# Kernel optimization log

Hardware: AMD Instinct MI355X
Metric: run time of the kernel (lower is better)

The kernel has to match this reference:

```python
import jax, jax.numpy as jnp
import numpy as np

D_MODEL, N_HEADS, D_HEAD, N_CTX, BATCH = 1024, 16, 64, 2048, 4
SCALED = True
NEG = 1e10


def setup_inputs() -> dict:
    key = jax.random.key(0)
    k1, k2, k3, k4 = jax.random.split(key, 4)
    s = 1.0 / np.sqrt(D_MODEL)
    return {
        "x": jax.random.normal(k1, (BATCH, N_CTX, D_MODEL), dtype=jnp.float32),
        "W_K": jax.random.normal(k2, (N_HEADS, D_HEAD, D_MODEL), dtype=jnp.float32) * s,
        "W_Q": jax.random.normal(k3, (N_HEADS, D_HEAD, D_MODEL), dtype=jnp.float32) * s,
        "W_V": jax.random.normal(k4, (N_HEADS, D_HEAD, D_MODEL), dtype=jnp.float32) * s,
    }


def reference(x, W_K, W_Q, W_V):
    b, p, _ = x.shape
    k = jnp.einsum('ihd,bpd->biph', W_K, x)
    q = jnp.einsum('ihd,bpd->biph', W_Q, x)
    v = jnp.einsum('ihd,bpd->biph', W_V, x)
    # attn_scores_pre: [b, i, q, p] (query axis named q, key axis p)
    scores = jnp.einsum('biph,biqh->biqp', k, q)
    mask = jnp.tril(jnp.ones((p, p), dtype=scores.dtype))
    scores = jnp.tril(scores) - NEG * (1.0 - mask)
    if SCALED:
        scores = scores / np.sqrt(D_HEAD)
    attn = jax.nn.softmax(scores, axis=-1)
    z = jnp.einsum('biph,biqp->biqh', v, attn)  # [b, i, q, h]
    out = jnp.transpose(z, (0, 2, 1, 3)).reshape(b, p, -1)  # b q (i h)
    return out
```

## Files before the change

### kernel.cpp

```cpp
#include <hip/hip_runtime.h>
#include <stdint.h>

typedef unsigned short u16;
typedef short bf16x8 __attribute__((ext_vector_type(8)));
typedef float f32x4 __attribute__((ext_vector_type(4)));
typedef u16 u16x8 __attribute__((ext_vector_type(8)));
typedef u16 u16x4 __attribute__((ext_vector_type(4)));
typedef uint32_t u32x2 __attribute__((ext_vector_type(2)));

#define NB 4
#define NH 16
#define NP 2048
#define NDM 1024
#define NEGBIG (-1e30f)
#define KLOG2E 0.18033688011112042f

__device__ __forceinline__ u16 f2bf(float f) {
    union { float f; uint32_t u; } v; v.f = f;
    return (u16)((v.u + 0x7FFFu + ((v.u >> 16) & 1u)) >> 16);
}

__device__ __forceinline__ uint32_t cvtpk_bf16(float lo, float hi) {
    uint32_t r;
    asm("v_cvt_pk_bf16_f32 %0, %1, %2" : "=v"(r) : "v"(lo), "v"(hi));
    return r;
}

__global__ void convert_x(const float* __restrict__ src, u16* __restrict__ dst, int n) {
    int i = (blockIdx.x * blockDim.x + threadIdx.x) * 4;
    int stride = gridDim.x * blockDim.x * 4;
    for (; i < n; i += stride) {
        float4 f = *(const float4*)(src + i);
        u16x4 o = { f2bf(f.x), f2bf(f.y), f2bf(f.z), f2bf(f.w) };
        *(u16x4*)(dst + i) = o;
    }
}

__global__ void convert_w(const float* __restrict__ wq, const float* __restrict__ wk,
                          const float* __restrict__ wv, u16* __restrict__ dst) {
    const int M = 1024 * 1024;
    int i = (blockIdx.x * blockDim.x + threadIdx.x) * 4;
    const float* src;
    float scale;
    if (i < M)            { src = wq + i;         scale = KLOG2E; }
    else if (i < 2 * M)   { src = wk + (i - M);   scale = 1.0f; }
    else                  { src = wv + (i - 2*M); scale = 1.0f; }
    float4 f = *(const float4*)src;
    u16x4 o = { f2bf(f.x * scale), f2bf(f.y * scale), f2bf(f.z * scale), f2bf(f.w * scale) };
    *(u16x4*)(dst + i) = o;
}

__device__ __forceinline__ void load_lds16(const void* g, void* l) {
    __builtin_amdgcn_global_load_lds(
        (const __attribute__((address_space(1))) uint32_t*)g,
        (__attribute__((address_space(3))) uint32_t*)l,
        16, 0, 0);
}

__global__ __launch_bounds__(256) void proj_gemm(
    const u16* __restrict__ xbf, const u16* __restrict__ wbf,
    u16* __restrict__ qws, u16* __restrict__ kws, u16* __restrict__ vtmp)
{
    __shared__ u16 As[128 * 64];
    __shared__ u16 Bs[128 * 64];
    int tid = threadIdx.x;
    int wave = tid >> 6, lane = tid & 63;
    int g = lane >> 4, c = lane & 15;
    int wr = wave >> 1, wc = wave & 1;
    int gx = blockIdx.x, gy = blockIdx.y;
    int wsel = gy >> 3;
    int n0 = (gy & 7) * 128;
    long m0 = (long)gx * 128;
    const u16* asrc0 = xbf + m0 * 1024;
    const u16* bsrc0 = wbf + (long)wsel * (1024 * 1024) + (long)n0 * 1024;

    int lrow = lane >> 3;
    int lcol = (lane & 7) * 8;

    f32x4 acc[4][4];
    #pragma unroll
    for (int i = 0; i < 4; i++)
        #pragma unroll
        for (int j = 0; j < 4; j++) acc[i][j] = (f32x4){0.f, 0.f, 0.f, 0.f};

    for (int kt = 0; kt < 16; kt++) {
        const u16* ak = asrc0 + kt * 64;
        const u16* bk_ = bsrc0 + kt * 64;
        #pragma unroll
        for (int r = 0; r < 4; r++) {
            int ldsoff = r * 2048 + wave * 512;
            int grow = r * 32 + wave * 8 + lrow;
            load_lds16(ak + (long)grow * 1024 + lcol, &As[ldsoff]);
            load_lds16(bk_ + (long)grow * 1024 + lcol, &Bs[ldsoff]);
        }
        __syncthreads();
        #pragma unroll
        for (int ks = 0; ks < 2; ks++) {
            bf16x8 af[4], bf_[4];
            #pragma unroll
            for (int mt = 0; mt < 4; mt++)
                af[mt] = *(const bf16x8*)&As[(wr * 64 + mt * 16 + c) * 64 + ks * 32 + g * 8];
            #pragma unroll
            for (int nt = 0; nt < 4; nt++)
                bf_[nt] = *(const bf16x8*)&Bs[(wc * 64 + nt * 16 + c) * 64 + ks * 32 + g * 8];
            #pragma unroll
            for (int mt = 0; mt < 4; mt++)
                #pragma unroll
                for (int nt = 0; nt < 4; nt++)
                    acc[mt][nt] = __builtin_amdgcn_mfma_f32_16x16x32_bf16(bf_[nt], af[mt], acc[mt][nt], 0, 0, 0);
        }
        __syncthreads();
    }

    u16* dst = (wsel == 0) ? qws : (wsel == 1) ? kws : vtmp;
    #pragma unroll
    for (int mt = 0; mt < 4; mt++) {
        #pragma unroll
        for (int nt = 0; nt < 4; nt++) {
            long m = m0 + wr * 64 + mt * 16 + c;
            int n_base = n0 + wc * 64 + nt * 16 + g * 4;
            int b = (int)(m >> 11), p = (int)(m & 2047);
            int hd = n_base >> 6, h = n_base & 63;
            u16x4 o;
            #pragma unroll
            for (int r = 0; r < 4; r++) o[r] = f2bf(acc[mt][nt][r]);
            *(u16x4*)(dst + ((((long)b * NH + hd) * NP + p) << 6) + h) = o;
        }
    }
}

__global__ __launch_bounds__(256) void transpose_v(const u16* __restrict__ src, u16* __restrict__ dst) {
    __shared__ u16 t[64][80];
    int tid = threadIdx.x;
    int bh = blockIdx.y;
    int p0 = blockIdx.x * 64;
    const u16* s = src + ((long)bh * NP + p0) * 64;
    #pragma unroll
    for (int rep = 0; rep < 2; rep++) {
        int pr = rep * 32 + (tid >> 3);
        int cc = (tid & 7) * 8;
        *(u16x8*)&t[pr][cc] = *(const u16x8*)(s + pr * 64 + cc);
    }
    __syncthreads();
    u16* d = dst + (long)bh * 64 * NP + p0;
    #pragma unroll
    for (int rep = 0; rep < 2; rep++) {
        int dh = rep * 32 + (tid >> 3);
        int pc = (tid & 7) * 8;
        u16x8 o;
        #pragma unroll
        for (int j = 0; j < 8; j++) o[j] = t[pc + j][dh];
        *(u16x8*)(d + (long)dh * NP + pc) = o;
    }
}

template<bool MASK>
__device__ __forceinline__ void attn_tile_lds(
    int kv0, const uint8_t* ldsK, const uint8_t* ldsV,
    const bf16x8 (&aq)[2][2], uint8_t* PwB, int c, int g, int q0,
    f32x4 (&acc_o)[2][4], float (&lrow)[2])
{
    int g4 = g * 4;
    int swz = (c & 7) << 4;

    f32x4 sa[2][4];
    __builtin_amdgcn_s_setprio(1);
    #pragma unroll
    for (int a = 0; a < 4; a++) {
        bf16x8 kf0 = *(const bf16x8*)(ldsK + (a * 16 + c) * 128 + ((g * 16) ^ swz));
        bf16x8 kf1 = *(const bf16x8*)(ldsK + (a * 16 + c) * 128 + ((64 + g * 16) ^ swz));
        #pragma unroll
        for (int mt = 0; mt < 2; mt++) {
            f32x4 z = (f32x4){0.f, 0.f, 0.f, 0.f};
            z = __builtin_amdgcn_mfma_f32_16x16x32_bf16(kf0, aq[mt][0], z, 0, 0, 0);
            z = __builtin_amdgcn_mfma_f32_16x16x32_bf16(kf1, aq[mt][1], z, 0, 0, 0);
            sa[mt][a] = z;
        }
    }
    __builtin_amdgcn_s_setprio(0);

    #pragma unroll
    for (int mt = 0; mt < 2; mt++) {
        float ps = 0.f;
        #pragma unroll
        for (int a = 0; a < 4; a++) {
            float p[4];
            #pragma unroll
            for (int r = 0; r < 4; r++) {
                p[r] = __builtin_amdgcn_exp2f(sa[mt][a][r] - 8.0f);
                if (MASK) {
                    int key = kv0 + a * 16 + g4 + r;
                    int qq = q0 + mt * 16 + c;
                    if (key > qq) p[r] = 0.f;
                }
                ps += p[r];
            }
            u32x2 wd = { cvtpk_bf16(p[0], p[1]), cvtpk_bf16(p[2], p[3]) };
            *(u32x2*)(PwB + c * 128 + ((a * 32 + g * 8) ^ swz)) = wd;
        }
        ps += __shfl_xor(ps, 16);
        ps += __shfl_xor(ps, 32);
        lrow[mt] += ps;

        __builtin_amdgcn_wave_barrier();

        __builtin_amdgcn_s_setprio(1);
        #pragma unroll
        for (int s = 0; s < 2; s++) {
            bf16x8 pa = *(const bf16x8*)(PwB + c * 128 + ((s * 64 + g * 16) ^ swz));
            #pragma unroll
            for (int j = 0; j < 4; j++) {
                bf16x8 bv = *(const bf16x8*)(ldsV + (j * 16 + c) * 128 + ((s * 64 + g * 16) ^ swz));
                acc_o[mt][j] = __builtin_amdgcn_mfma_f32_16x16x32_bf16(pa, bv, acc_o[mt][j], 0, 0, 0);
            }
        }
        __builtin_amdgcn_s_setprio(0);
        __builtin_amdgcn_wave_barrier();
    }
}

__global__ __launch_bounds__(512, 4) void attn_kernel(
    const u16* __restrict__ qws, const u16* __restrict__ kws,
    const u16* __restrict__ vT, float* __restrict__ out)
{
    __shared__ __align__(16) uint8_t smem[65536];
    int tid = threadIdx.x;
    int wave = tid >> 6, lane = tid & 63;
    int c = lane & 15, g = lane >> 4;
    int xs = blockIdx.x >> 6;
    int qb = (xs < 4) ? (7 - 2 * xs) : (2 * (xs - 4));
    int bh = blockIdx.x & 63;
    int q0 = qb * 256 + wave * 32;
    const u16* qp = qws + (long)bh * NP * 64;
    const uint8_t* kb = (const uint8_t*)(kws + (long)bh * NP * 64);
    const uint8_t* vb = (const uint8_t*)(vT + (long)bh * 64 * NP);
    uint8_t* PwB = smem + 49152 + wave * 2048;

    bf16x8 aq[2][2];
    #pragma unroll
    for (int mt = 0; mt < 2; mt++)
        #pragma unroll
        for (int s = 0; s < 2; s++)
            aq[mt][s] = *(const bf16x8*)(qp + (long)(q0 + mt * 16 + c) * 64 + s * 32 + g * 8);

    f32x4 acc_o[2][4];
    float lrow[2] = {0.f, 0.f};
    #pragma unroll
    for (int mt = 0; mt < 2; mt++)
        #pragma unroll
        for (int j = 0; j < 4; j++) acc_o[mt][j] = (f32x4){0.f, 0.f, 0.f, 0.f};

    int r3 = lane >> 3;
    int cb = ((lane & 7) ^ r3) << 4;
    int srow = wave * 8 + r3;

    int myTmax = (q0 + 31) >> 6;
    int Tblk = qb * 4 + 3;

    auto stage = [&](int t) {
        uint8_t* dst = smem + (t % 3) * 16384;
        int kv = t * 64;
        load_lds16(kb + (size_t)(kv + srow) * 128 + cb, dst + wave * 1024);
        load_lds16(vb + (size_t)srow * (NP * 2) + (size_t)kv * 2 + cb, dst + 8192 + wave * 1024);
    };

    stage(0);
    stage(1);
    asm volatile("s_waitcnt vmcnt(2)" ::: "memory");
    __builtin_amdgcn_sched_barrier(0);
    __builtin_amdgcn_s_barrier();
    __builtin_amdgcn_sched_barrier(0);

    for (int t = 0; t <= Tblk; t++) {
        if (t + 2 <= Tblk) stage(t + 2);
        if (t <= myTmax) {
            const uint8_t* ldsK = smem + (t % 3) * 16384;
            const uint8_t* ldsV = ldsK + 8192;
            if (t == myTmax)
                attn_tile_lds<true>(t * 64, ldsK, ldsV, aq, PwB, c, g, q0, acc_o, lrow);
            else
                attn_tile_lds<false>(t * 64, ldsK, ldsV, aq, PwB, c, g, q0, acc_o, lrow);
        }
        asm volatile("s_waitcnt vmcnt(2)" ::: "memory");
        __builtin_amdgcn_sched_barrier(0);
        __builtin_amdgcn_s_barrier();
        __builtin_amdgcn_sched_barrier(0);
    }

    int b = bh >> 4, hh = bh & 15;
    #pragma unroll
    for (int mt = 0; mt < 2; mt++) {
        float invc = 1.0f / lrow[mt];
        #pragma unroll
        for (int r = 0; r < 4; r++) {
            float li = __shfl(invc, g * 4 + r);
            int qq = q0 + mt * 16 + g * 4 + r;
            #pragma unroll
            for (int j = 0; j < 4; j++)
                out[((long)b * NP + qq) * 1024 + hh * 64 + j * 16 + c] = acc_o[mt][j][r] * li;
        }
    }
}

extern "C" void kernel_launch(void* const* d_in, const int* in_sizes, int n_in,
                              void* d_out, int out_size, void* d_ws, size_t ws_size,
                              hipStream_t stream) {
    const float* x  = (const float*)d_in[0];
    const float* wk = (const float*)d_in[1];
    const float* wq = (const float*)d_in[2];
    const float* wv = (const float*)d_in[3];

    uint8_t* ws = (uint8_t*)d_ws;
    u16* x_bf  = (u16*)(ws + 0);
    u16* w_bf  = (u16*)(ws + (16u << 20));
    u16* q_ws  = (u16*)(ws + (22u << 20));
    u16* k_ws  = (u16*)(ws + (38u << 20));
    u16* vtmp  = (u16*)(ws + (54u << 20));
    u16* v_wsT = (u16*)(ws + 0);

    convert_x<<<2048, 256, 0, stream>>>(x, x_bf, NB * NP * NDM);
    convert_w<<<3072, 256, 0, stream>>>(wq, wk, wv, w_bf);

    proj_gemm<<<dim3(64, 24), 256, 0, stream>>>(x_bf, w_bf, q_ws, k_ws, vtmp);
    transpose_v<<<dim3(32, 64), 256, 0, stream>>>(vtmp, v_wsT);
    attn_kernel<<<512, 512, 0, stream>>>(q_ws, k_ws, v_wsT, (float*)d_out);
}
```

Baseline: 189.3 us.

## Fuse conversions, write V transposed from GEMM, and load attention K/V from global

The two fp32→bf16 conversion kernels are merged into a single launch. The V projection epilogue now writes V already transposed, so the separate transpose kernel goes away. The attention kernel drops its shared-memory triple-buffered K/V pipeline: each wave reads K and V straight from global memory and keeps only a per-wave P buffer with a new swizzle. Blocks shrink to 4 waves over 128 query rows with a new causal balancing order. This cuts launches and a V round trip, but adds scalar, uncoalesced V stores in the GEMM and loses K/V reuse across waves in LDS.

Result: slower. 227.5 us (+20.2%).

```diff
diff --git a/kernel.cpp b/kernel.cpp
--- a/kernel.cpp
+++ b/kernel.cpp
@@ -12,7 +12,6 @@
 #define NH 16
 #define NP 2048
 #define NDM 1024
-#define NEGBIG (-1e30f)
 #define KLOG2E 0.18033688011112042f
 
 __device__ __forceinline__ u16 f2bf(float f) {
@@ -26,28 +25,24 @@
     return r;
 }
 
-__global__ void convert_x(const float* __restrict__ src, u16* __restrict__ dst, int n) {
+__global__ void convert_all(const float* __restrict__ x, const float* __restrict__ wq,
+                            const float* __restrict__ wk, const float* __restrict__ wv,
+                            u16* __restrict__ x_bf, u16* __restrict__ w_bf) {
+    const int XT = NB * NP * NDM;
+    const int M1 = NDM * NDM;
     int i = (blockIdx.x * blockDim.x + threadIdx.x) * 4;
-    int stride = gridDim.x * blockDim.x * 4;
-    for (; i < n; i += stride) {
-        float4 f = *(const float4*)(src + i);
-        u16x4 o = { f2bf(f.x), f2bf(f.y), f2bf(f.z), f2bf(f.w) };
-        *(u16x4*)(dst + i) = o;
-    }
-}
-
-__global__ void convert_w(const float* __restrict__ wq, const float* __restrict__ wk,
-                          const float* __restrict__ wv, u16* __restrict__ dst) {
-    const int M = 1024 * 1024;
-    int i = (blockIdx.x * blockDim.x + threadIdx.x) * 4;
-    const float* src;
-    float scale;
-    if (i < M)            { src = wq + i;         scale = KLOG2E; }
-    else if (i < 2 * M)   { src = wk + (i - M);   scale = 1.0f; }
-    else                  { src = wv + (i - 2*M); scale = 1.0f; }
+    const float* src; u16* dst; float scale = 1.0f;
+    if (i < XT) { src = x + i; dst = x_bf + i; }
+    else {
+        int j = i - XT;
+        dst = w_bf + j;
+        if (j < M1)          { src = wq + j;          scale = KLOG2E; }
+        else if (j < 2 * M1) { src = wk + (j - M1); }
+        else                 { src = wv + (j - 2 * M1); }
+    }
     float4 f = *(const float4*)src;
     u16x4 o = { f2bf(f.x * scale), f2bf(f.y * scale), f2bf(f.z * scale), f2bf(f.w * scale) };
-    *(u16x4*)(dst + i) = o;
+    *(u16x4*)dst = o;
 }
 
 __device__ __forceinline__ void load_lds16(const void* g, void* l) {
@@ -59,7 +54,7 @@
 
 __global__ __launch_bounds__(256) void proj_gemm(
     const u16* __restrict__ xbf, const u16* __restrict__ wbf,
-    u16* __restrict__ qws, u16* __restrict__ kws, u16* __restrict__ vtmp)
+    u16* __restrict__ qws, u16* __restrict__ kws, u16* __restrict__ vT)
 {
     __shared__ u16 As[128 * 64];
     __shared__ u16 Bs[128 * 64];
@@ -112,129 +107,124 @@
         __syncthreads();
     }
 
-    u16* dst = (wsel == 0) ? qws : (wsel == 1) ? kws : vtmp;
-    #pragma unroll
-    for (int mt = 0; mt < 4; mt++) {
-        #pragma unroll
-        for (int nt = 0; nt < 4; nt++) {
+    if (wsel < 2) {
+        u16* dst = (wsel == 0) ? qws : kws;
+        #pragma unroll
+        for (int mt = 0; mt < 4; mt++) {
+            #pragma unroll
+            for (int nt = 0; nt < 4; nt++) {
+                long m = m0 + wr * 64 + mt * 16 + c;
+                int n_base = n0 + wc * 64 + nt * 16 + g * 4;
+                int b = (int)(m >> 11), p = (int)(m & 2047);
+                int hd = n_base >> 6, h = n_base & 63;
+                u16x4 o;
+                #pragma unroll
+                for (int r = 0; r < 4; r++) o[r] = f2bf(acc[mt][nt][r]);
+                *(u16x4*)(dst + ((((long)b * NH + hd) * NP + p) << 6) + h) = o;
+            }
+        }
+    } else {
+        #pragma unroll
+        for (int mt = 0; mt < 4; mt++) {
             long m = m0 + wr * 64 + mt * 16 + c;
-            int n_base = n0 + wc * 64 + nt * 16 + g * 4;
             int b = (int)(m >> 11), p = (int)(m & 2047);
-            int hd = n_base >> 6, h = n_base & 63;
-            u16x4 o;
-            #pragma unroll
-            for (int r = 0; r < 4; r++) o[r] = f2bf(acc[mt][nt][r]);
-            *(u16x4*)(dst + ((((long)b * NH + hd) * NP + p) << 6) + h) = o;
-        }
-    }
-}
-
-__global__ __launch_bounds__(256) void transpose_v(const u16* __restrict__ src, u16* __restrict__ dst) {
-    __shared__ u16 t[64][80];
-    int tid = threadIdx.x;
-    int bh = blockIdx.y;
-    int p0 = blockIdx.x * 64;
-    const u16* s = src + ((long)bh * NP + p0) * 64;
-    #pragma unroll
-    for (int rep = 0; rep < 2; rep++) {
-        int pr = rep * 32 + (tid >> 3);
-        int cc = (tid & 7) * 8;
-        *(u16x8*)&t[pr][cc] = *(const u16x8*)(s + pr * 64 + cc);
-    }
-    __syncthreads();
-    u16* d = dst + (long)bh * 64 * NP + p0;
-    #pragma unroll
-    for (int rep = 0; rep < 2; rep++) {
-        int dh = rep * 32 + (tid >> 3);
-        int pc = (tid & 7) * 8;
-        u16x8 o;
-        #pragma unroll
-        for (int j = 0; j < 8; j++) o[j] = t[pc + j][dh];
-        *(u16x8*)(d + (long)dh * NP + pc) = o;
+            #pragma unroll
+            for (int nt = 0; nt < 4; nt++) {
+                int n_base = n0 + wc * 64 + nt * 16 + g * 4;
+                #pragma unroll
+                for (int r = 0; r < 4; r++)
+                    vT[((long)b * 1024 + n_base + r) * NP + p] = f2bf(acc[mt][nt][r]);
+            }
+        }
     }
 }
 
 template<bool MASK>
-__device__ __forceinline__ void attn_tile_lds(
-    int kv0, const uint8_t* ldsK, const uint8_t* ldsV,
-    const bf16x8 (&aq)[2][2], uint8_t* PwB, int c, int g, int q0,
+__device__ __forceinline__ void attn_tile(
+    int kv0, const u16* __restrict__ kp, const u16* __restrict__ vp,
+    const bf16x8 (&aq)[2][2], uint8_t* PwB, int c, int g, int sx, int q0,
     f32x4 (&acc_o)[2][4], float (&lrow)[2])
 {
-    int g4 = g * 4;
-    int swz = (c & 7) << 4;
-
-    f32x4 sa[2][4];
-    __builtin_amdgcn_s_setprio(1);
+    float ps[2] = {0.f, 0.f};
     #pragma unroll
     for (int a = 0; a < 4; a++) {
-        bf16x8 kf0 = *(const bf16x8*)(ldsK + (a * 16 + c) * 128 + ((g * 16) ^ swz));
-        bf16x8 kf1 = *(const bf16x8*)(ldsK + (a * 16 + c) * 128 + ((64 + g * 16) ^ swz));
+        const u16* kr = kp + (size_t)(kv0 + a * 16 + c) * 64 + g * 8;
+        bf16x8 kf0 = *(const bf16x8*)(kr);
+        bf16x8 kf1 = *(const bf16x8*)(kr + 32);
         #pragma unroll
         for (int mt = 0; mt < 2; mt++) {
             f32x4 z = (f32x4){0.f, 0.f, 0.f, 0.f};
             z = __builtin_amdgcn_mfma_f32_16x16x32_bf16(kf0, aq[mt][0], z, 0, 0, 0);
             z = __builtin_amdgcn_mfma_f32_16x16x32_bf16(kf1, aq[mt][1], z, 0, 0, 0);
-            sa[mt][a] = z;
-        }
-    }
-    __builtin_amdgcn_s_setprio(0);
-
-    #pragma unroll
-    for (int mt = 0; mt < 2; mt++) {
-        float ps = 0.f;
-        #pragma unroll
-        for (int a = 0; a < 4; a++) {
             float p[4];
             #pragma unroll
             for (int r = 0; r < 4; r++) {
-                p[r] = __builtin_amdgcn_exp2f(sa[mt][a][r] - 8.0f);
+                p[r] = __builtin_amdgcn_exp2f(z[r] - 8.0f);
                 if (MASK) {
-                    int key = kv0 + a * 16 + g4 + r;
+                    int key = kv0 + a * 16 + g * 4 + r;
                     int qq = q0 + mt * 16 + c;
                     if (key > qq) p[r] = 0.f;
                 }
-                ps += p[r];
+                ps[mt] += p[r];
             }
             u32x2 wd = { cvtpk_bf16(p[0], p[1]), cvtpk_bf16(p[2], p[3]) };
-            *(u32x2*)(PwB + c * 128 + ((a * 32 + g * 8) ^ swz)) = wd;
-        }
-        ps += __shfl_xor(ps, 16);
-        ps += __shfl_xor(ps, 32);
-        lrow[mt] += ps;
-
-        __builtin_amdgcn_wave_barrier();
-
-        __builtin_amdgcn_s_setprio(1);
-        #pragma unroll
-        for (int s = 0; s < 2; s++) {
-            bf16x8 pa = *(const bf16x8*)(PwB + c * 128 + ((s * 64 + g * 16) ^ swz));
-            #pragma unroll
-            for (int j = 0; j < 4; j++) {
-                bf16x8 bv = *(const bf16x8*)(ldsV + (j * 16 + c) * 128 + ((s * 64 + g * 16) ^ swz));
-                acc_o[mt][j] = __builtin_amdgcn_mfma_f32_16x16x32_bf16(pa, bv, acc_o[mt][j], 0, 0, 0);
-            }
-        }
-        __builtin_amdgcn_s_setprio(0);
-        __builtin_amdgcn_wave_barrier();
-    }
-}
-
-__global__ __launch_bounds__(512, 4) void attn_kernel(
+            *(u32x2*)(PwB + (mt * 16 + c) * 128 + ((a * 32 + g * 8) ^ sx)) = wd;
+        }
+    }
+
+    bf16x8 bv0[4];
+    #pragma unroll
+    for (int j = 0; j < 4; j++)
+        bv0[j] = *(const bf16x8*)(vp + (size_t)(j * 16 + c) * NP + kv0 + g * 8);
+
+    #pragma unroll
+    for (int mt = 0; mt < 2; mt++) {
+        float p = ps[mt];
+        p += __shfl_xor(p, 16);
+        p += __shfl_xor(p, 32);
+        lrow[mt] += p;
+    }
+
+    __builtin_amdgcn_wave_barrier();
+
+    bf16x8 pa0 = *(const bf16x8*)(PwB + (0 * 16 + c) * 128 + ((0 + g * 16) ^ sx));
+    bf16x8 pa1 = *(const bf16x8*)(PwB + (1 * 16 + c) * 128 + ((0 + g * 16) ^ sx));
+    bf16x8 bv1[4];
+    #pragma unroll
+    for (int j = 0; j < 4; j++)
+        bv1[j] = *(const bf16x8*)(vp + (size_t)(j * 16 + c) * NP + kv0 + 32 + g * 8);
+    #pragma unroll
+    for (int j = 0; j < 4; j++) {
+        acc_o[0][j] = __builtin_amdgcn_mfma_f32_16x16x32_bf16(pa0, bv0[j], acc_o[0][j], 0, 0, 0);
+        acc_o[1][j] = __builtin_amdgcn_mfma_f32_16x16x32_bf16(pa1, bv0[j], acc_o[1][j], 0, 0, 0);
+    }
+    pa0 = *(const bf16x8*)(PwB + (0 * 16 + c) * 128 + ((64 + g * 16) ^ sx));
+    pa1 = *(const bf16x8*)(PwB + (1 * 16 + c) * 128 + ((64 + g * 16) ^ sx));
+    #pragma unroll
+    for (int j = 0; j < 4; j++) {
+        acc_o[0][j] = __builtin_amdgcn_mfma_f32_16x16x32_bf16(pa0, bv1[j], acc_o[0][j], 0, 0, 0);
+        acc_o[1][j] = __builtin_amdgcn_mfma_f32_16x16x32_bf16(pa1, bv1[j], acc_o[1][j], 0, 0, 0);
+    }
+    __builtin_amdgcn_wave_barrier();
+}
+
+__global__ __launch_bounds__(256, 4) void attn_kernel(
     const u16* __restrict__ qws, const u16* __restrict__ kws,
     const u16* __restrict__ vT, float* __restrict__ out)
 {
-    __shared__ __align__(16) uint8_t smem[65536];
+    __shared__ __align__(16) uint8_t Plds[16384];
     int tid = threadIdx.x;
     int wave = tid >> 6, lane = tid & 63;
     int c = lane & 15, g = lane >> 4;
     int xs = blockIdx.x >> 6;
-    int qb = (xs < 4) ? (7 - 2 * xs) : (2 * (xs - 4));
+    int qb = (xs < 4) ? (15 - xs) : (xs < 8) ? (xs + 4) : (xs < 12) ? (xs - 4) : (15 - xs);
     int bh = blockIdx.x & 63;
-    int q0 = qb * 256 + wave * 32;
+    int q0 = qb * 128 + wave * 32;
     const u16* qp = qws + (long)bh * NP * 64;
-    const uint8_t* kb = (const uint8_t*)(kws + (long)bh * NP * 64);
-    const uint8_t* vb = (const uint8_t*)(vT + (long)bh * 64 * NP);
-    uint8_t* PwB = smem + 49152 + wave * 2048;
+    const u16* kp = kws + (long)bh * NP * 64;
+    const u16* vp = vT + (long)bh * 64 * NP;
+    uint8_t* PwB = Plds + wave * 4096;
+    int sx = ((c & 7) << 4) ^ ((c & 8) << 3);
 
     bf16x8 aq[2][2];
     #pragma unroll
@@ -250,42 +240,10 @@
         #pragma unroll
         for (int j = 0; j < 4; j++) acc_o[mt][j] = (f32x4){0.f, 0.f, 0.f, 0.f};
 
-    int r3 = lane >> 3;
-    int cb = ((lane & 7) ^ r3) << 4;
-    int srow = wave * 8 + r3;
-
-    int myTmax = (q0 + 31) >> 6;
-    int Tblk = qb * 4 + 3;
-
-    auto stage = [&](int t) {
-        uint8_t* dst = smem + (t % 3) * 16384;
-        int kv = t * 64;
-        load_lds16(kb + (size_t)(kv + srow) * 128 + cb, dst + wave * 1024);
-        load_lds16(vb + (size_t)srow * (NP * 2) + (size_t)kv * 2 + cb, dst + 8192 + wave * 1024);
-    };
-
-    stage(0);
-    stage(1);
-    asm volatile("s_waitcnt vmcnt(2)" ::: "memory");
-    __builtin_amdgcn_sched_barrier(0);
-    __builtin_amdgcn_s_barrier();
-    __builtin_amdgcn_sched_barrier(0);
-
-    for (int t = 0; t <= Tblk; t++) {
-        if (t + 2 <= Tblk) stage(t + 2);
-        if (t <= myTmax) {
-            const uint8_t* ldsK = smem + (t % 3) * 16384;
-            const uint8_t* ldsV = ldsK + 8192;
-            if (t == myTmax)
-                attn_tile_lds<true>(t * 64, ldsK, ldsV, aq, PwB, c, g, q0, acc_o, lrow);
-            else
-                attn_tile_lds<false>(t * 64, ldsK, ldsV, aq, PwB, c, g, q0, acc_o, lrow);
-        }
-        asm volatile("s_waitcnt vmcnt(2)" ::: "memory");
-        __builtin_amdgcn_sched_barrier(0);
-        __builtin_amdgcn_s_barrier();
-        __builtin_amdgcn_sched_barrier(0);
-    }
+    int tmax = (q0 + 31) >> 6;
+    for (int t = 0; t < tmax; t++)
+        attn_tile<false>(t * 64, kp, vp, aq, PwB, c, g, sx, q0, acc_o, lrow);
+    attn_tile<true>(tmax * 64, kp, vp, aq, PwB, c, g, sx, q0, acc_o, lrow);
 
     int b = bh >> 4, hh = bh & 15;
     #pragma unroll
@@ -311,17 +269,13 @@
     const float* wv = (const float*)d_in[3];
 
     uint8_t* ws = (uint8_t*)d_ws;
-    u16* x_bf  = (u16*)(ws + 0);
-    u16* w_bf  = (u16*)(ws + (16u << 20));
-    u16* q_ws  = (u16*)(ws + (22u << 20));
-    u16* k_ws  = (u16*)(ws + (38u << 20));
-    u16* vtmp  = (u16*)(ws + (54u << 20));
-    u16* v_wsT = (u16*)(ws + 0);
-
-    convert_x<<<2048, 256, 0, stream>>>(x, x_bf, NB * NP * NDM);
-    convert_w<<<3072, 256, 0, stream>>>(wq, wk, wv, w_bf);
-
-    proj_gemm<<<dim3(64, 24), 256, 0, stream>>>(x_bf, w_bf, q_ws, k_ws, vtmp);
-    transpose_v<<<dim3(32, 64), 256, 0, stream>>>(vtmp, v_wsT);
-    attn_kernel<<<512, 512, 0, stream>>>(q_ws, k_ws, v_wsT, (float*)d_out);
-}
+    u16* x_bf = (u16*)(ws + 0);
+    u16* w_bf = (u16*)(ws + (16u << 20));
+    u16* q_ws = (u16*)(ws + (22u << 20));
+    u16* k_ws = (u16*)(ws + (38u << 20));
+    u16* v_wsT = (u16*)(ws + (54u << 20));
+
+    convert_all<<<11264, 256, 0, stream>>>(x, wq, wk, wv, x_bf, w_bf);
+    proj_gemm<<<dim3(64, 24), 256, 0, stream>>>(x_bf, w_bf, q_ws, k_ws, v_wsT);
+    attn_kernel<<<1024, 256, 0, stream>>>(q_ws, k_ws, v_wsT, (float*)d_out);
+}
```
